# Optimization experiments

Measured on AMD Instinct MI355X. Metric: run time of the kernel, lower is better.

Reference implementation:

```python
import jax, jax.numpy as jnp
import numpy as np
import math

N_HEADS = 16
HEAD_DIM = 64
D_MODEL = 1024
B, S = 2, 2048


def setup_inputs() -> dict:
    key = jax.random.key(0)
    ks = jax.random.split(key, 12)
    Dh = N_HEADS * HEAD_DIM
    sc = 1.0 / math.sqrt(D_MODEL)
    return {
        "will_be_queries": jax.random.normal(ks[0], (B, S, D_MODEL), jnp.float32),
        "will_be_keys": jax.random.normal(ks[1], (B, S, D_MODEL), jnp.float32),
        "will_be_values": jax.random.normal(ks[2], (B, S, D_MODEL), jnp.float32),
        "valid_len": jax.random.randint(ks[3], (B,), 1, S + 1, jnp.int32),
        # torch nn.Linear weights: (out_features, in_features)
        "w_q": jax.random.normal(ks[4], (Dh, D_MODEL), jnp.float32) * sc,
        "b_q": jnp.zeros((Dh,), jnp.float32),
        "w_k": jax.random.normal(ks[5], (Dh, D_MODEL), jnp.float32) * sc,
        "b_k": jnp.zeros((Dh,), jnp.float32),
        "w_v": jax.random.normal(ks[6], (Dh, D_MODEL), jnp.float32) * sc,
        "b_v": jnp.zeros((Dh,), jnp.float32),
        "w_o": jax.random.normal(ks[7], (D_MODEL, Dh), jnp.float32) * sc,
        "b_o": jnp.zeros((D_MODEL,), jnp.float32),
    }


def _split_heads(x):
    # (B, S, H*Dh) -> (B, H, S, Dh)
    b, s, _ = x.shape
    return x.reshape(b, s, N_HEADS, HEAD_DIM).transpose(0, 2, 1, 3)


def reference(will_be_queries, will_be_keys, will_be_values, valid_len,
              w_q, b_q, w_k, b_k, w_v, b_v, w_o, b_o):
    q = _split_heads(will_be_queries @ w_q.T + b_q)   # (B,H,S,Dh)
    k = _split_heads(will_be_keys @ w_k.T + b_k)
    v = _split_heads(will_be_values @ w_v.T + b_v)

    scores = jnp.einsum("bhqd,bhkd->bhqk", q, k) / jnp.sqrt(
        jnp.asarray(HEAD_DIM, q.dtype))

    neg = jnp.finfo(scores.dtype).min
    q_idx = jnp.arange(scores.shape[2])[:, None]   # (S,1)
    k_idx = jnp.arange(scores.shape[3])[None, :]   # (1,S)
    causal = k_idx > q_idx                         # look-ahead mask (offset=1 triu)
    vmask = k_idx[None] >= valid_len[:, None, None]  # (B,S,S) keys beyond valid_len
    mask = causal[None, None] | vmask[:, None]       # (B,1|H,S,S) broadcast over heads
    scores = jnp.where(mask, neg, scores)

    attn = jax.nn.softmax(scores, axis=-1)
    out = jnp.einsum("bhqk,bhkd->bhqd", attn, v)   # (B,H,S,Dh)
    out = out.transpose(0, 2, 1, 3).reshape(out.shape[0], out.shape[2], N_HEADS * HEAD_DIM)
    return out @ w_o.T + b_o
```

## Files before the change

kernel.cpp:

```cpp
#include <hip/hip_runtime.h>
#include <math.h>

#define NH 16
#define HD 64
#define DM 1024
#define BB 2
#define SS 2048
#define MROWS (BB*SS)
#define MEG 1048576

typedef __attribute__((ext_vector_type(8))) short bf16x8;
typedef __attribute__((ext_vector_type(4))) float f32x4;

__device__ __forceinline__ unsigned short f2bf(float x) {
    unsigned int u = __float_as_uint(x);
    u += 0x7fff + ((u >> 16) & 1);
    return (unsigned short)(u >> 16);
}

#define GLD_LDS16(gp, lp) __builtin_amdgcn_global_load_lds(                  \
        (const __attribute__((address_space(1))) void*)(gp),                 \
        (__attribute__((address_space(3))) void*)(lp), 16, 0, 0)

__global__ __launch_bounds__(256)
void cvt_all(const float* __restrict__ xq, const float* __restrict__ xk,
             const float* __restrict__ xv, const float* __restrict__ wq,
             const float* __restrict__ wk, const float* __restrict__ wv,
             const float* __restrict__ wo, unsigned short* __restrict__ ws)
{
    const int reg = blockIdx.y;
    const size_t n    = (reg < 3) ? (size_t)4 * MEG : (size_t)MEG;
    const size_t roff = (reg < 3) ? (size_t)reg * 4 * MEG
                                  : (size_t)12 * MEG + (size_t)(reg - 3) * MEG;
    const float* src = (reg == 0) ? xq : (reg == 1) ? xk : (reg == 2) ? xv :
                       (reg == 3) ? wq : (reg == 4) ? wk : (reg == 5) ? wv : wo;
    const size_t i = ((size_t)blockIdx.x * 256 + threadIdx.x) * 8;
    if (i >= n) return;
    const float4 a = *(const float4*)(src + i);
    const float4 b = *(const float4*)(src + i + 4);
    ushort4 lo4, hi4;
    lo4.x = f2bf(a.x); lo4.y = f2bf(a.y); lo4.z = f2bf(a.z); lo4.w = f2bf(a.w);
    hi4.x = f2bf(b.x); hi4.y = f2bf(b.y); hi4.z = f2bf(b.z); hi4.w = f2bf(b.w);
    *(ushort4*)(ws + roff + i)     = lo4;
    *(ushort4*)(ws + roff + i + 4) = hi4;
}

template<int MODE>
__device__ __forceinline__ void gemm_mfma_core(
    const unsigned short* __restrict__ A,
    const unsigned short* __restrict__ W,
    const float* __restrict__ bias,
    void* __restrict__ Y, int ldy)
{
    __shared__ unsigned short As[128 * 64];
    __shared__ unsigned short Bs[128 * 64];

    const int tid  = threadIdx.x;
    const int w    = tid >> 6;
    const int lane = tid & 63;
    const int lo   = lane & 15;
    const int g    = lane >> 4;
    const int wr   = (w >> 1) * 64;
    const int wc   = (w & 1) * 64;

    f32x4 acc[4][4];
#pragma unroll
    for (int i = 0; i < 4; ++i)
#pragma unroll
        for (int j = 0; j < 4; ++j) acc[i][j] = (f32x4)0.f;

    for (int k0 = 0; k0 < 1024; k0 += 64) {
        __syncthreads();
#pragma unroll
        for (int u = 0; u < 4; ++u) {
            const int e   = (u * 256 + tid) * 8;
            const int row = e >> 6, col = e & 63;
            GLD_LDS16(A + (size_t)row * 1024 + k0 + col, As + e);
            GLD_LDS16(W + (size_t)row * 1024 + k0 + col, Bs + e);
        }
        asm volatile("s_waitcnt vmcnt(0)" ::: "memory");
        __syncthreads();

#pragma unroll
        for (int kk = 0; kk < 2; ++kk) {
            bf16x8 af[4], bf[4];
#pragma unroll
            for (int i = 0; i < 4; ++i) {
                af[i] = *(const bf16x8*)(As + (wr + i * 16 + lo) * 64 + kk * 32 + g * 8);
                bf[i] = *(const bf16x8*)(Bs + (wc + i * 16 + lo) * 64 + kk * 32 + g * 8);
            }
#pragma unroll
            for (int i = 0; i < 4; ++i)
#pragma unroll
                for (int j = 0; j < 4; ++j)
                    acc[i][j] = __builtin_amdgcn_mfma_f32_16x16x32_bf16(
                        af[i], bf[j], acc[i][j], 0, 0, 0);
        }
    }

#pragma unroll
    for (int i = 0; i < 4; ++i) {
#pragma unroll
        for (int j = 0; j < 4; ++j) {
            const int col = wc + j * 16 + lo;
#pragma unroll
            for (int r = 0; r < 4; ++r) {
                const int row = wr + i * 16 + g * 4 + r;
                if constexpr (MODE == 2) {
                    const float v = acc[i][j][r] + bias[row];
                    const int jc = (col & ~63) | ((((col >> 3) & 7) ^ (row & 7)) << 3)
                                 | (col & 7);
                    ((unsigned short*)Y)[(size_t)row * ldy + jc] = f2bf(v);
                } else {
                    const float v = acc[i][j][r] + bias[col];
                    if constexpr (MODE == 0)
                        ((unsigned short*)Y)[(size_t)row * ldy + col] = f2bf(v);
                    else
                        ((float*)Y)[(size_t)row * ldy + col] = v;
                }
            }
        }
    }
}

__global__ __launch_bounds__(256)
void qkv_proj(const unsigned short* __restrict__ ws,
              const float* __restrict__ bq, const float* __restrict__ bk,
              const float* __restrict__ bv,
              unsigned short* __restrict__ qk, unsigned short* __restrict__ vt)
{
    const int nblk = blockIdx.x;
    if (nblk < 16) {
        const int mat  = nblk >> 3;
        const int ncol = (nblk & 7) * 128;
        const int m0   = blockIdx.y * 128;
        const unsigned short* A = ws + (size_t)mat * 4 * MEG + (size_t)m0 * 1024;
        const unsigned short* W = ws + (size_t)12 * MEG + (size_t)mat * MEG
                                     + (size_t)ncol * 1024;
        const float* bias = ((mat == 0) ? bq : bk) + ncol;
        gemm_mfma_core<0>(A, W, bias,
                          qk + (size_t)m0 * 2048 + mat * 1024 + ncol, 2048);
    } else {
        const int rowblk = nblk - 16;
        const int b      = blockIdx.y >> 4;
        const int colblk = blockIdx.y & 15;
        const unsigned short* A = ws + (size_t)14 * MEG + (size_t)rowblk * 128 * 1024;
        const unsigned short* W = ws + (size_t)8 * MEG + (size_t)b * 2 * MEG
                                     + (size_t)colblk * 128 * 1024;
        gemm_mfma_core<2>(A, W, bv + rowblk * 128,
                          vt + (size_t)b * 1024 * 2048
                             + (size_t)rowblk * 128 * 2048 + colblk * 128, 2048);
    }
}

__global__ __launch_bounds__(256)
void out_proj(const unsigned short* __restrict__ ws,
              const float* __restrict__ bo, float* __restrict__ out)
{
    const int n0 = blockIdx.x * 128;
    const int m0 = blockIdx.y * 128;
    const unsigned short* A = ws + (size_t)28 * MEG + (size_t)m0 * 1024;
    const unsigned short* W = ws + (size_t)15 * MEG + (size_t)n0 * 1024;
    gemm_mfma_core<1>(A, W, bo + n0, out + (size_t)m0 * 1024 + n0, 1024);
}

__global__ __launch_bounds__(256)
void attn_mfma(const unsigned short* __restrict__ qk,
               const unsigned short* __restrict__ vt,
               const int* __restrict__ vlen, unsigned short* __restrict__ aout)
{
    __shared__ unsigned short Ks[2][64 * 64];
    __shared__ unsigned short Vs[2][64 * 64];
    __shared__ unsigned short Ps[4][16][72];

    const int bh  = blockIdx.x;
    const int pr  = blockIdx.y;
    const int b   = bh >> 4;
    const int h   = bh & 15;
    const int vl  = vlen[b];
    const int tid = threadIdx.x;
    const int w    = tid >> 6;
    const int lane = tid & 63;
    const int lo   = lane & 15;
    const int g    = lane >> 4;

    const unsigned short* qbase = qk + (size_t)(b * SS) * 2048 + h * 64;
    const unsigned short* kbase = qbase + 1024;
    const unsigned short* vtb   = vt + (size_t)b * 1024 * 2048
                                     + (size_t)(h * 64) * 2048;

#pragma unroll
    for (int half = 0; half < 2; ++half) {
        const int qt = half ? (31 - pr) : pr;
        const int q0 = qt * 64;
        const int qg = q0 + w * 16 + lo;

        const bf16x8 a0 = *(const bf16x8*)(qbase + (size_t)qg * 2048 + g * 8);
        const bf16x8 a1 = *(const bf16x8*)(qbase + (size_t)qg * 2048 + 32 + g * 8);

        float mR = -INFINITY, lR = 0.f;
        f32x4 of[4];
#pragma unroll
        for (int f = 0; f < 4; ++f) of[f] = (f32x4)0.f;

        const int kmax   = min(q0 + 64, vl);
        const int ntiles = (kmax + 63) >> 6;

#pragma unroll
        for (int u = 0; u < 2; ++u) {
            const int e = w * 128 + u * 64 + lane;
            const int r = e >> 3, c = e & 7;
            GLD_LDS16(kbase + (size_t)r * 2048 + ((c ^ (r & 7)) * 8),
                      &Ks[0][e * 8]);
            GLD_LDS16(vtb + (size_t)r * 2048 + c * 8, &Vs[0][e * 8]);
        }

        for (int kt = 0; kt < ntiles; ++kt) {
            const int cur = kt & 1;
            const int k0  = kt * 64;
            if (kt + 1 < ntiles) {
                const int kn = k0 + 64;
#pragma unroll
                for (int u = 0; u < 2; ++u) {
                    const int e = w * 128 + u * 64 + lane;
                    const int r = e >> 3, c = e & 7;
                    GLD_LDS16(kbase + (size_t)(kn + r) * 2048 + ((c ^ (r & 7)) * 8),
                              &Ks[cur ^ 1][e * 8]);
                    GLD_LDS16(vtb + (size_t)r * 2048 + kn + c * 8,
                              &Vs[cur ^ 1][e * 8]);
                }
                asm volatile("s_waitcnt vmcnt(4)" ::: "memory");
            } else {
                asm volatile("s_waitcnt vmcnt(0)" ::: "memory");
            }
            __syncthreads();

            f32x4 sf[4];
#pragma unroll
            for (int f = 0; f < 4; ++f) sf[f] = (f32x4)0.f;
#pragma unroll
            for (int f = 0; f < 4; ++f) {
                const int kr = f * 16 + lo;
                const bf16x8 kb0 = *(const bf16x8*)(&Ks[cur][kr * 64 + ((g ^ (lo & 7)) * 8)]);
                const bf16x8 kb1 = *(const bf16x8*)(&Ks[cur][kr * 64 + (((4 + g) ^ (lo & 7)) * 8)]);
                sf[f] = __builtin_amdgcn_mfma_f32_16x16x32_bf16(kb0, a0, sf[f], 0, 0, 0);
                sf[f] = __builtin_amdgcn_mfma_f32_16x16x32_bf16(kb1, a1, sf[f], 0, 0, 0);
            }

            const bool full = (k0 + 63 <= q0 + w * 16) && (k0 + 64 <= vl);
            float sv[16];
            float t = -INFINITY;
#pragma unroll
            for (int f = 0; f < 4; ++f)
#pragma unroll
                for (int r = 0; r < 4; ++r) {
                    float x = sf[f][r] * 0.125f;
                    if (!full) {
                        const int kg = k0 + f * 16 + g * 4 + r;
                        x = (kg <= qg && kg < vl) ? x : -INFINITY;
                    }
                    sv[f * 4 + r] = x;
                    t = fmaxf(t, x);
                }
            t = fmaxf(t, __shfl_xor(t, 16));
            t = fmaxf(t, __shfl_xor(t, 32));
            const float mn   = fmaxf(mR, t);
            const float corr = __expf(mR - mn);
            float ps = 0.f;
#pragma unroll
            for (int f = 0; f < 4; ++f) {
                const float p0 = __expf(sv[f * 4 + 0] - mn);
                const float p1 = __expf(sv[f * 4 + 1] - mn);
                const float p2 = __expf(sv[f * 4 + 2] - mn);
                const float p3 = __expf(sv[f * 4 + 3] - mn);
                ps += (p0 + p1) + (p2 + p3);
                ushort4 pk;
                pk.x = f2bf(p0); pk.y = f2bf(p1); pk.z = f2bf(p2); pk.w = f2bf(p3);
                *(ushort4*)&Ps[w][lo][f * 16 + g * 4] = pk;
            }
            ps += __shfl_xor(ps, 16);
            ps += __shfl_xor(ps, 32);
            lR = lR * corr + ps;
            mR = mn;

            float crs[4];
#pragma unroll
            for (int r = 0; r < 4; ++r) crs[r] = __shfl(corr, g * 4 + r);
#pragma unroll
            for (int f = 0; f < 4; ++f)
#pragma unroll
                for (int r = 0; r < 4; ++r) of[f][r] *= crs[r];

#pragma unroll
            for (int kk = 0; kk < 2; ++kk) {
                const bf16x8 pa = *(const bf16x8*)&Ps[w][lo][kk * 32 + g * 8];
#pragma unroll
                for (int f = 0; f < 4; ++f) {
                    const bf16x8 vb = *(const bf16x8*)(&Vs[cur][(f * 16 + lo) * 64
                                        + (((4 * kk + g) ^ (lo & 7)) * 8)]);
                    of[f] = __builtin_amdgcn_mfma_f32_16x16x32_bf16(pa, vb, of[f], 0, 0, 0);
                }
            }
            __syncthreads();
        }

        float rv[4];
#pragma unroll
        for (int r = 0; r < 4; ++r) rv[r] = 1.0f / __shfl(lR, g * 4 + r);
        unsigned short* ob = aout + (size_t)(b * SS + q0 + w * 16) * 1024 + h * 64;
#pragma unroll
        for (int f = 0; f < 4; ++f)
#pragma unroll
            for (int r = 0; r < 4; ++r)
                ob[(size_t)(g * 4 + r) * 1024 + f * 16 + lo] = f2bf(of[f][r] * rv[r]);
    }
}

extern "C" void kernel_launch(void* const* d_in, const int* in_sizes, int n_in,
                              void* d_out, int out_size, void* d_ws, size_t ws_size,
                              hipStream_t stream) {
    const float* xq = (const float*)d_in[0];
    const float* xk = (const float*)d_in[1];
    const float* xv = (const float*)d_in[2];
    const int*   vl = (const int*)  d_in[3];
    const float* wq = (const float*)d_in[4];
    const float* bq = (const float*)d_in[5];
    const float* wk = (const float*)d_in[6];
    const float* bk = (const float*)d_in[7];
    const float* wv = (const float*)d_in[8];
    const float* bv = (const float*)d_in[9];
    const float* wo = (const float*)d_in[10];
    const float* bo = (const float*)d_in[11];

    unsigned short* ws     = (unsigned short*)d_ws;
    unsigned short* qkbuf  = ws + (size_t)16 * MEG;
    unsigned short* vtbuf  = ws + (size_t)24 * MEG;
    unsigned short* abuf   = ws + (size_t)28 * MEG;

    cvt_all<<<dim3(2048, 7), 256, 0, stream>>>(xq, xk, xv, wq, wk, wv, wo, ws);
    qkv_proj<<<dim3(24, 32), 256, 0, stream>>>(ws, bq, bk, bv, qkbuf, vtbuf);
    attn_mfma<<<dim3(BB * NH, 16), 256, 0, stream>>>(qkbuf, vtbuf, vl, abuf);
    out_proj<<<dim3(8, 32), 256, 0, stream>>>(ws, bo, (float*)d_out);
}
```

Before: 150.6 us.

## Split attention into one q-tile per block, lazy rescale, transposed PV MFMA

Each attention block now handles a single 64-row query tile, longest tiles launched first, instead of pairing a light and a heavy tile per block. This doubles the grid and relies on the hardware scheduler for load balance. The online softmax skips rescaling the accumulator unless the running max grows by more than 8, and the PV MFMA operands are swapped so each lane holds a whole output row. That removes the corr shuffles and allows vectorized ushort4 stores. The P buffer uses an XOR-swizzled layout, and s_setprio is raised around the MFMA sections to favour matrix work across waves.

```diff
diff --git a/kernel.cpp b/kernel.cpp
--- a/kernel.cpp
+++ b/kernel.cpp
@@ -171,148 +171,152 @@
 {
     __shared__ unsigned short Ks[2][64 * 64];
     __shared__ unsigned short Vs[2][64 * 64];
-    __shared__ unsigned short Ps[4][16][72];
+    __shared__ unsigned short Ps[4][16 * 64];
 
     const int bh  = blockIdx.x;
-    const int pr  = blockIdx.y;
+    const int qt  = 31 - blockIdx.y;
     const int b   = bh >> 4;
     const int h   = bh & 15;
+    const int q0  = qt * 64;
     const int vl  = vlen[b];
     const int tid = threadIdx.x;
     const int w    = tid >> 6;
     const int lane = tid & 63;
     const int lo   = lane & 15;
     const int g    = lane >> 4;
+    const int lx   = lo & 7;
 
     const unsigned short* qbase = qk + (size_t)(b * SS) * 2048 + h * 64;
     const unsigned short* kbase = qbase + 1024;
     const unsigned short* vtb   = vt + (size_t)b * 1024 * 2048
                                      + (size_t)(h * 64) * 2048;
 
-#pragma unroll
-    for (int half = 0; half < 2; ++half) {
-        const int qt = half ? (31 - pr) : pr;
-        const int q0 = qt * 64;
-        const int qg = q0 + w * 16 + lo;
-
-        const bf16x8 a0 = *(const bf16x8*)(qbase + (size_t)qg * 2048 + g * 8);
-        const bf16x8 a1 = *(const bf16x8*)(qbase + (size_t)qg * 2048 + 32 + g * 8);
-
-        float mR = -INFINITY, lR = 0.f;
-        f32x4 of[4];
-#pragma unroll
-        for (int f = 0; f < 4; ++f) of[f] = (f32x4)0.f;
-
-        const int kmax   = min(q0 + 64, vl);
-        const int ntiles = (kmax + 63) >> 6;
-
-#pragma unroll
-        for (int u = 0; u < 2; ++u) {
-            const int e = w * 128 + u * 64 + lane;
-            const int r = e >> 3, c = e & 7;
-            GLD_LDS16(kbase + (size_t)r * 2048 + ((c ^ (r & 7)) * 8),
-                      &Ks[0][e * 8]);
-            GLD_LDS16(vtb + (size_t)r * 2048 + c * 8, &Vs[0][e * 8]);
-        }
-
-        for (int kt = 0; kt < ntiles; ++kt) {
-            const int cur = kt & 1;
-            const int k0  = kt * 64;
-            if (kt + 1 < ntiles) {
-                const int kn = k0 + 64;
-#pragma unroll
-                for (int u = 0; u < 2; ++u) {
-                    const int e = w * 128 + u * 64 + lane;
-                    const int r = e >> 3, c = e & 7;
-                    GLD_LDS16(kbase + (size_t)(kn + r) * 2048 + ((c ^ (r & 7)) * 8),
-                              &Ks[cur ^ 1][e * 8]);
-                    GLD_LDS16(vtb + (size_t)r * 2048 + kn + c * 8,
-                              &Vs[cur ^ 1][e * 8]);
+    const int qg = q0 + w * 16 + lo;
+    const bf16x8 a0 = *(const bf16x8*)(qbase + (size_t)qg * 2048 + g * 8);
+    const bf16x8 a1 = *(const bf16x8*)(qbase + (size_t)qg * 2048 + 32 + g * 8);
+
+    float mR = -INFINITY, lR = 0.f;
+    f32x4 of[4];
+#pragma unroll
+    for (int f = 0; f < 4; ++f) of[f] = (f32x4)0.f;
+
+    const int kmax   = min(q0 + 64, vl);
+    const int ntiles = (kmax + 63) >> 6;
+
+#pragma unroll
+    for (int u = 0; u < 2; ++u) {
+        const int e = w * 128 + u * 64 + lane;
+        const int r = e >> 3, c = e & 7;
+        GLD_LDS16(kbase + (size_t)r * 2048 + ((c ^ (r & 7)) * 8), &Ks[0][e * 8]);
+        GLD_LDS16(vtb + (size_t)r * 2048 + c * 8, &Vs[0][e * 8]);
+    }
+
+    unsigned short* const Psw = Ps[w];
+
+    for (int kt = 0; kt < ntiles; ++kt) {
+        const int cur = kt & 1;
+        const int k0  = kt * 64;
+        if (kt + 1 < ntiles) {
+            const int kn = k0 + 64;
+#pragma unroll
+            for (int u = 0; u < 2; ++u) {
+                const int e = w * 128 + u * 64 + lane;
+                const int r = e >> 3, c = e & 7;
+                GLD_LDS16(kbase + (size_t)(kn + r) * 2048 + ((c ^ (r & 7)) * 8),
+                          &Ks[cur ^ 1][e * 8]);
+                GLD_LDS16(vtb + (size_t)r * 2048 + kn + c * 8, &Vs[cur ^ 1][e * 8]);
+            }
+            asm volatile("s_waitcnt vmcnt(4)" ::: "memory");
+        } else {
+            asm volatile("s_waitcnt vmcnt(0)" ::: "memory");
+        }
+        __syncthreads();
+
+        f32x4 sf[4];
+#pragma unroll
+        for (int f = 0; f < 4; ++f) sf[f] = (f32x4)0.f;
+        __builtin_amdgcn_s_setprio(1);
+#pragma unroll
+        for (int f = 0; f < 4; ++f) {
+            const int kr = f * 16 + lo;
+            const bf16x8 kb0 = *(const bf16x8*)(&Ks[cur][kr * 64 + ((g ^ lx) * 8)]);
+            const bf16x8 kb1 = *(const bf16x8*)(&Ks[cur][kr * 64 + (((4 + g) ^ lx) * 8)]);
+            sf[f] = __builtin_amdgcn_mfma_f32_16x16x32_bf16(kb0, a0, sf[f], 0, 0, 0);
+            sf[f] = __builtin_amdgcn_mfma_f32_16x16x32_bf16(kb1, a1, sf[f], 0, 0, 0);
+        }
+        __builtin_amdgcn_s_setprio(0);
+
+        const bool full = (k0 + 63 <= q0 + w * 16) && (k0 + 64 <= vl);
+        float sv[16];
+        float t = -INFINITY;
+#pragma unroll
+        for (int f = 0; f < 4; ++f)
+#pragma unroll
+            for (int r = 0; r < 4; ++r) {
+                float x = sf[f][r] * 0.125f;
+                if (!full) {
+                    const int kg = k0 + f * 16 + g * 4 + r;
+                    x = (kg <= qg && kg < vl) ? x : -INFINITY;
                 }
-                asm volatile("s_waitcnt vmcnt(4)" ::: "memory");
-            } else {
-                asm volatile("s_waitcnt vmcnt(0)" ::: "memory");
-            }
-            __syncthreads();
-
-            f32x4 sf[4];
-#pragma unroll
-            for (int f = 0; f < 4; ++f) sf[f] = (f32x4)0.f;
-#pragma unroll
-            for (int f = 0; f < 4; ++f) {
-                const int kr = f * 16 + lo;
-                const bf16x8 kb0 = *(const bf16x8*)(&Ks[cur][kr * 64 + ((g ^ (lo & 7)) * 8)]);
-                const bf16x8 kb1 = *(const bf16x8*)(&Ks[cur][kr * 64 + (((4 + g) ^ (lo & 7)) * 8)]);
-                sf[f] = __builtin_amdgcn_mfma_f32_16x16x32_bf16(kb0, a0, sf[f], 0, 0, 0);
-                sf[f] = __builtin_amdgcn_mfma_f32_16x16x32_bf16(kb1, a1, sf[f], 0, 0, 0);
-            }
-
-            const bool full = (k0 + 63 <= q0 + w * 16) && (k0 + 64 <= vl);
-            float sv[16];
-            float t = -INFINITY;
-#pragma unroll
-            for (int f = 0; f < 4; ++f)
-#pragma unroll
-                for (int r = 0; r < 4; ++r) {
-                    float x = sf[f][r] * 0.125f;
-                    if (!full) {
-                        const int kg = k0 + f * 16 + g * 4 + r;
-                        x = (kg <= qg && kg < vl) ? x : -INFINITY;
-                    }
-                    sv[f * 4 + r] = x;
-                    t = fmaxf(t, x);
-                }
-            t = fmaxf(t, __shfl_xor(t, 16));
-            t = fmaxf(t, __shfl_xor(t, 32));
+                sv[f * 4 + r] = x;
+                t = fmaxf(t, x);
+            }
+        t = fmaxf(t, __shfl_xor(t, 16));
+        t = fmaxf(t, __shfl_xor(t, 32));
+
+        if (!__all(t <= mR + 8.f)) {
             const float mn   = fmaxf(mR, t);
             const float corr = __expf(mR - mn);
-            float ps = 0.f;
+            lR *= corr;
+#pragma unroll
+            for (int f = 0; f < 4; ++f)
+#pragma unroll
+                for (int r = 0; r < 4; ++r) of[f][r] *= corr;
+            mR = mn;
+        }
+
+        float ps = 0.f;
+#pragma unroll
+        for (int f = 0; f < 4; ++f) {
+            const float p0 = __expf(sv[f * 4 + 0] - mR);
+            const float p1 = __expf(sv[f * 4 + 1] - mR);
+            const float p2 = __expf(sv[f * 4 + 2] - mR);
+            const float p3 = __expf(sv[f * 4 + 3] - mR);
+            ps += (p0 + p1) + (p2 + p3);
+            ushort4 pk;
+            pk.x = f2bf(p0); pk.y = f2bf(p1); pk.z = f2bf(p2); pk.w = f2bf(p3);
+            *(ushort4*)(Psw + lo * 64 + (((f * 2 + (g >> 1)) ^ lx) * 8)
+                        + (g & 1) * 4) = pk;
+        }
+        ps += __shfl_xor(ps, 16);
+        ps += __shfl_xor(ps, 32);
+        lR += ps;
+
+        __builtin_amdgcn_s_setprio(1);
+#pragma unroll
+        for (int kk = 0; kk < 2; ++kk) {
+            const bf16x8 pa = *(const bf16x8*)(Psw + lo * 64 + (((kk * 4 + g) ^ lx) * 8));
 #pragma unroll
             for (int f = 0; f < 4; ++f) {
-                const float p0 = __expf(sv[f * 4 + 0] - mn);
-                const float p1 = __expf(sv[f * 4 + 1] - mn);
-                const float p2 = __expf(sv[f * 4 + 2] - mn);
-                const float p3 = __expf(sv[f * 4 + 3] - mn);
-                ps += (p0 + p1) + (p2 + p3);
-                ushort4 pk;
-                pk.x = f2bf(p0); pk.y = f2bf(p1); pk.z = f2bf(p2); pk.w = f2bf(p3);
-                *(ushort4*)&Ps[w][lo][f * 16 + g * 4] = pk;
-            }
-            ps += __shfl_xor(ps, 16);
-            ps += __shfl_xor(ps, 32);
-            lR = lR * corr + ps;
-            mR = mn;
-
-            float crs[4];
-#pragma unroll
-            for (int r = 0; r < 4; ++r) crs[r] = __shfl(corr, g * 4 + r);
-#pragma unroll
-            for (int f = 0; f < 4; ++f)
-#pragma unroll
-                for (int r = 0; r < 4; ++r) of[f][r] *= crs[r];
-
-#pragma unroll
-            for (int kk = 0; kk < 2; ++kk) {
-                const bf16x8 pa = *(const bf16x8*)&Ps[w][lo][kk * 32 + g * 8];
-#pragma unroll
-                for (int f = 0; f < 4; ++f) {
-                    const bf16x8 vb = *(const bf16x8*)(&Vs[cur][(f * 16 + lo) * 64
-                                        + (((4 * kk + g) ^ (lo & 7)) * 8)]);
-                    of[f] = __builtin_amdgcn_mfma_f32_16x16x32_bf16(pa, vb, of[f], 0, 0, 0);
-                }
-            }
-            __syncthreads();
-        }
-
-        float rv[4];
-#pragma unroll
-        for (int r = 0; r < 4; ++r) rv[r] = 1.0f / __shfl(lR, g * 4 + r);
-        unsigned short* ob = aout + (size_t)(b * SS + q0 + w * 16) * 1024 + h * 64;
-#pragma unroll
-        for (int f = 0; f < 4; ++f)
-#pragma unroll
-            for (int r = 0; r < 4; ++r)
-                ob[(size_t)(g * 4 + r) * 1024 + f * 16 + lo] = f2bf(of[f][r] * rv[r]);
+                const bf16x8 vb = *(const bf16x8*)(&Vs[cur][(f * 16 + lo) * 64
+                                    + (((4 * kk + g) ^ lx) * 8)]);
+                of[f] = __builtin_amdgcn_mfma_f32_16x16x32_bf16(vb, pa, of[f], 0, 0, 0);
+            }
+        }
+        __builtin_amdgcn_s_setprio(0);
+        __syncthreads();
+    }
+
+    const float rv = 1.0f / lR;
+    unsigned short* ob = aout + (size_t)(b * SS + q0 + w * 16 + lo) * 1024 + h * 64;
+#pragma unroll
+    for (int f = 0; f < 4; ++f) {
+        ushort4 ov;
+        ov.x = f2bf(of[f][0] * rv);
+        ov.y = f2bf(of[f][1] * rv);
+        ov.z = f2bf(of[f][2] * rv);
+        ov.w = f2bf(of[f][3] * rv);
+        *(ushort4*)(ob + f * 16 + g * 4) = ov;
     }
 }
 
@@ -339,6 +343,6 @@
 
     cvt_all<<<dim3(2048, 7), 256, 0, stream>>>(xq, xk, xv, wq, wk, wv, wo, ws);
     qkv_proj<<<dim3(24, 32), 256, 0, stream>>>(ws, bq, bk, bv, qkbuf, vtbuf);
-    attn_mfma<<<dim3(BB * NH, 16), 256, 0, stream>>>(qkbuf, vtbuf, vl, abuf);
+    attn_mfma<<<dim3(BB * NH, SS / 64), 256, 0, stream>>>(qkbuf, vtbuf, vl, abuf);
     out_proj<<<dim3(8, 32), 256, 0, stream>>>(ws, bo, (float*)d_out);
 }
```

Result: faster. 138.0 us (-8.3%).
